# Optimization experiments

Hardware: AMD Instinct MI355X
Metric: run time of the kernel (lower is better)

The kernel has to match this reference:

```python
import jax, jax.numpy as jnp
import numpy as np


def setup_inputs() -> dict:
    key = jax.random.key(0)
    ks = jax.random.split(key, 5)
    b, t, q_dim, kv_dim, h = 16, 128, 256, 64, 4
    c = t - 1
    q_x = jax.random.normal(ks[0], (b, t, q_dim), dtype=jnp.float32)
    kv_x = jax.random.normal(ks[1], (b, t, c, kv_dim), dtype=jnp.float32)
    # Linear weights stored as [in, out]; no biases (bias=False in torch module).
    sq = 1.0 / np.sqrt(q_dim)
    sk = 1.0 / np.sqrt(kv_dim)
    Wq = jax.random.uniform(ks[2], (q_dim, kv_dim * h), jnp.float32, -sq, sq)
    Wk = jax.random.uniform(ks[3], (kv_dim, kv_dim * h), jnp.float32, -sk, sk)
    Wv = jax.random.uniform(ks[4], (kv_dim, kv_dim * h), jnp.float32, -sk, sk)
    return {"q_x": q_x, "kv_x": kv_x, "Wq": Wq, "Wk": Wk, "Wv": Wv}


def reference(q_x, kv_x, Wq, Wk, Wv):
    b, t, c, k = kv_x.shape  # c = t - 1
    h = Wq.shape[1] // k
    # projections
    q = (q_x @ Wq).reshape(b, t, h, k)          # [b,t,h,k]
    keys = (kv_x @ Wk).reshape(b, t, c, h, k)   # [b,t,c,h,k]
    vals = (kv_x @ Wv).reshape(b, t, c, h, k)
    # per-token attention over the c-sized context
    scores = jnp.einsum('bthk,btchk->bthc', q, keys) / jnp.sqrt(jnp.float32(k))
    w = jax.nn.softmax(scores, axis=-1)          # softmax over context dim
    out = jnp.einsum('bthc,btchk->bthk', w, vals)
    return out.reshape(b, t, h * k)
```

## Files before the change

### kernel.cpp

```cpp
#include <hip/hip_runtime.h>
#include <math.h>

#define Bdim 16
#define Tdim 128
#define Cdim 127
#define Hdim 4
#define QD   256
#define HK   256

#define DPP_XOR1        0xB1
#define DPP_XOR2        0x4E
#define DPP_HALF_MIRROR 0x141
#define DPP_MIRROR      0x140
template<int CTRL>
__device__ __forceinline__ float dpp_movf(float x) {
    return __int_as_float(__builtin_amdgcn_update_dpp(
        0, __float_as_int(x), CTRL, 0xF, 0xF, true));
}

__global__ __launch_bounds__(256) void precompute_M(
        const float* __restrict__ Wq, const float* __restrict__ Wk,
        float* __restrict__ M) {
    __shared__ float wk_s[64][129];
    __shared__ float wq_s[2][128];
    int I = blockIdx.x;
    int H = blockIdx.y;
    int tid = threadIdx.x;

    #pragma unroll
    for (int it = 0; it < 8; ++it) {
        int flat = tid + it * 256;
        int m = flat >> 5, kq = flat & 31;
        float4 v = *(const float4*)(Wk + m * HK + H * 128 + kq * 4);
        wk_s[m][kq*4+0] = v.x; wk_s[m][kq*4+1] = v.y;
        wk_s[m][kq*4+2] = v.z; wk_s[m][kq*4+3] = v.w;
    }
    if (tid < 64) {
        int r = tid >> 5, kq = tid & 31;
        float4 v = *(const float4*)(Wq + (size_t)(I*2+r) * HK + H * 128 + kq * 4);
        wq_s[r][kq*4+0] = v.x; wq_s[r][kq*4+1] = v.y;
        wq_s[r][kq*4+2] = v.z; wq_s[r][kq*4+3] = v.w;
    }
    __syncthreads();

    int r = tid >> 7, hh = (tid >> 6) & 1, m = tid & 63;
    float acc = 0.f;
    #pragma unroll 8
    for (int j = 0; j < 64; ++j)
        acc = fmaf(wq_s[r][hh*64+j], wk_s[m][hh*64+j], acc);
    M[(size_t)(I*2+r) * HK + H * 128 + hh * 64 + m] = acc;
}

template <int NS>
__global__ __launch_bounds__(256) void qk_gemm(
        const float* __restrict__ q_x,
        const float* __restrict__ M,
        float* __restrict__ part) {
    const int KLEN = 256 / NS;
    __shared__ __align__(16) float q_s[16][256 / NS];
    int RB = blockIdx.x;
    int S  = blockIdx.y;
    int tid = threadIdx.x;

    for (int f = tid; f < 16 * KLEN / 4; f += 256) {
        int r = f / (KLEN / 4), kq = f % (KLEN / 4);
        *(float4*)&q_s[r][kq*4] =
            *(const float4*)(q_x + (size_t)(RB*16 + r) * QD + S * KLEN + kq * 4);
    }
    __syncthreads();

    float acc[16];
    #pragma unroll
    for (int r = 0; r < 16; ++r) acc[r] = 0.f;

    for (int kk = 0; kk < KLEN / 4; ++kk) {
        int k = S * KLEN + kk * 4;
        float m0 = M[(size_t)(k+0) * HK + tid];
        float m1 = M[(size_t)(k+1) * HK + tid];
        float m2 = M[(size_t)(k+2) * HK + tid];
        float m3 = M[(size_t)(k+3) * HK + tid];
        #pragma unroll
        for (int r = 0; r < 16; ++r) {
            float4 qv = *(const float4*)&q_s[r][kk*4];
            acc[r] = fmaf(qv.x, m0, fmaf(qv.y, m1, fmaf(qv.z, m2, fmaf(qv.w, m3, acc[r]))));
        }
    }
    float* dst = part + (size_t)S * (Bdim*Tdim*HK) + (size_t)RB * 16 * HK + tid;
    #pragma unroll
    for (int r = 0; r < 16; ++r) dst[r * HK] = acc[r];
}

__global__ __launch_bounds__(512, 8) void attn_main(
        const float* __restrict__ kv_x,
        const float* __restrict__ qk_p, int nsplit,
        const float* __restrict__ Wv,
        float* __restrict__ out) {
    __shared__ __align__(16) float4 sX4[128 * 16];
    __shared__ __align__(16) float qk_s[HK];
    __shared__ __align__(16) float e_lds[128 * 5 + 4];
    __shared__ __align__(16) float4 wx4[Hdim * 16];
    __shared__ float red_max[Hdim][2];
    __shared__ float red_sum[Hdim][2];

    int bt  = blockIdx.x;
    int tid = threadIdx.x;

    const float4* Xg = (const float4*)(kv_x + (size_t)bt * (Cdim * 64));
    #pragma unroll
    for (int it = 0; it < 4; ++it) {
        int l = tid + it * 512;
        if (l < Cdim * 16) {
            int c = l >> 4, p = l & 15;
            __builtin_amdgcn_global_load_lds(
                (const __attribute__((address_space(1))) void*)(Xg + (c << 4) + (p ^ (c & 7))),
                (__attribute__((address_space(3))) void*)(sX4 + l), 16, 0, 0);
        }
    }
    if (tid >= 256 && tid < 320)
        ((float*)sX4)[Cdim * 64 + (tid - 256)] = 0.f;
    if (tid < 256) {
        float q = 0.f;
        for (int s = 0; s < nsplit; ++s)
            q += qk_p[(size_t)s * (Bdim*Tdim*HK) + (size_t)bt * HK + tid];
        qk_s[tid] = q;
    }
    __syncthreads();

    int h    = tid >> 7;
    int c    = tid & 127;
    int half = (tid >> 6) & 1;
    int lane = tid & 63;
    int sw   = c & 7;

    float s;
    {
        const float4* qrow = (const float4*)(qk_s + h * 64);
        const float4* xrow = sX4 + c * 16;
        float acc = 0.f;
        #pragma unroll
        for (int p = 0; p < 16; ++p) {
            float4 qv = qrow[p];
            float4 x4 = xrow[p ^ sw];
            acc = fmaf(qv.x, x4.x, fmaf(qv.y, x4.y, fmaf(qv.z, x4.z, fmaf(qv.w, x4.w, acc))));
        }
        s = (c < Cdim) ? acc * 0.125f : -INFINITY;
    }

    float mx = s;
    mx = fmaxf(mx, dpp_movf<DPP_XOR1>(mx));
    mx = fmaxf(mx, dpp_movf<DPP_XOR2>(mx));
    mx = fmaxf(mx, dpp_movf<DPP_HALF_MIRROR>(mx));
    mx = fmaxf(mx, dpp_movf<DPP_MIRROR>(mx));
    mx = fmaxf(mx, __shfl_xor(mx, 16, 64));
    mx = fmaxf(mx, __shfl_xor(mx, 32, 64));
    if (lane == 0) red_max[h][half] = mx;
    __syncthreads();
    float gm = fmaxf(red_max[h][0], red_max[h][1]);
    float e = __expf(s - gm);
    e_lds[c * 5 + h] = e;
    float sm = e;
    sm += dpp_movf<DPP_XOR1>(sm);
    sm += dpp_movf<DPP_XOR2>(sm);
    sm += dpp_movf<DPP_HALF_MIRROR>(sm);
    sm += dpp_movf<DPP_MIRROR>(sm);
    sm += __shfl_xor(sm, 16, 64);
    sm += __shfl_xor(sm, 32, 64);
    if (lane == 0) red_sum[h][half] = sm;
    __syncthreads();

    {
        int jc = (tid >> 3) & 15;
        int cs = tid & 7;
        const float4* xbase = sX4 + cs * 16 + (jc ^ cs);
        const float* ebase  = e_lds + cs * 5 + h;
        float4 a = {0.f, 0.f, 0.f, 0.f};
        #pragma unroll
        for (int m = 0; m < 16; ++m) {
            float4 x4 = xbase[m * 128];
            float ev  = ebase[m * 40];
            a.x = fmaf(ev, x4.x, a.x);
            a.y = fmaf(ev, x4.y, a.y);
            a.z = fmaf(ev, x4.z, a.z);
            a.w = fmaf(ev, x4.w, a.w);
        }
        a.x += dpp_movf<DPP_XOR1>(a.x); a.y += dpp_movf<DPP_XOR1>(a.y);
        a.z += dpp_movf<DPP_XOR1>(a.z); a.w += dpp_movf<DPP_XOR1>(a.w);
        a.x += dpp_movf<DPP_XOR2>(a.x); a.y += dpp_movf<DPP_XOR2>(a.y);
        a.z += dpp_movf<DPP_XOR2>(a.z); a.w += dpp_movf<DPP_XOR2>(a.w);
        a.x += dpp_movf<DPP_HALF_MIRROR>(a.x); a.y += dpp_movf<DPP_HALF_MIRROR>(a.y);
        a.z += dpp_movf<DPP_HALF_MIRROR>(a.z); a.w += dpp_movf<DPP_HALF_MIRROR>(a.w);
        if (cs == 0) wx4[h * 16 + jc] = a;
    }
    __syncthreads();

    if (tid < 256) {
        int hh = tid >> 6, k = tid & 63;
        float inv = 1.f / (red_sum[hh][0] + red_sum[hh][1]);
        const float* wvcol = Wv + hh * 64 + k;
        float acc = 0.f;
        #pragma unroll 4
        for (int jc = 0; jc < 16; ++jc) {
            float4 w4 = wx4[hh * 16 + jc];
            acc = fmaf(w4.x, wvcol[(size_t)(jc*4+0) * HK], acc);
            acc = fmaf(w4.y, wvcol[(size_t)(jc*4+1) * HK], acc);
            acc = fmaf(w4.z, wvcol[(size_t)(jc*4+2) * HK], acc);
            acc = fmaf(w4.w, wvcol[(size_t)(jc*4+3) * HK], acc);
        }
        out[(size_t)bt * HK + tid] = acc * inv;
    }
}

extern "C" void kernel_launch(void* const* d_in, const int* in_sizes, int n_in,
                              void* d_out, int out_size, void* d_ws, size_t ws_size,
                              hipStream_t stream) {
    const float* q_x  = (const float*)d_in[0];
    const float* kv_x = (const float*)d_in[1];
    const float* Wq   = (const float*)d_in[2];
    const float* Wk   = (const float*)d_in[3];
    const float* Wv   = (const float*)d_in[4];
    float* out = (float*)d_out;

    float* M     = (float*)d_ws;
    float* parts = M + 256 * 256;

    size_t need4 = (size_t)(256*256 + 4 * Bdim*Tdim*HK) * sizeof(float);
    int nsplit = (ws_size >= need4) ? 4 : 1;

    precompute_M<<<dim3(128, 2), 256, 0, stream>>>(Wq, Wk, M);
    if (nsplit == 4)
        qk_gemm<4><<<dim3(128, 4), 256, 0, stream>>>(q_x, M, parts);
    else
        qk_gemm<1><<<dim3(128, 1), 256, 0, stream>>>(q_x, M, parts);
    attn_main<<<Bdim * Tdim, 512, 0, stream>>>(kv_x, parts, nsplit, Wv, out);
}
```

Before: 42.05 us.

## Make attention blocks persistent over four tokens with double-buffered LDS prefetch

Each attention block now handles four consecutive (b,t) tokens and prefetches the next token's kv_x tile into a second LDS buffer while it computes the current one. The qk partial sums are prefetched into registers. The upper 256 threads keep their Wv column in 64 registers across iterations, so Wv is read once per block. The goal is to hide global-load latency, amortise Wv loads and cut the block count. The costs are higher register use (launch bounds drop to 4 blocks), double the LDS footprint, manual waitcnt/barrier scheduling that is fragile, and fewer blocks (512), which may leave CUs underfilled.

```diff
diff --git a/kernel.cpp b/kernel.cpp
--- a/kernel.cpp
+++ b/kernel.cpp
@@ -7,6 +7,9 @@
 #define Hdim 4
 #define QD   256
 #define HK   256
+#define BT   (Bdim * Tdim)
+#define ITERS 4
+#define NBLK  (BT / ITERS)
 
 #define DPP_XOR1        0xB1
 #define DPP_XOR2        0x4E
@@ -85,46 +88,57 @@
             acc[r] = fmaf(qv.x, m0, fmaf(qv.y, m1, fmaf(qv.z, m2, fmaf(qv.w, m3, acc[r]))));
         }
     }
-    float* dst = part + (size_t)S * (Bdim*Tdim*HK) + (size_t)RB * 16 * HK + tid;
+    float* dst = part + (size_t)S * (BT*HK) + (size_t)RB * 16 * HK + tid;
     #pragma unroll
     for (int r = 0; r < 16; ++r) dst[r * HK] = acc[r];
 }
 
-__global__ __launch_bounds__(512, 8) void attn_main(
+__device__ __forceinline__ void stage_x(const float4* __restrict__ Xg,
+                                        float4* dst, int tid) {
+    #pragma unroll
+    for (int itr = 0; itr < 4; ++itr) {
+        int l = tid + itr * 512;
+        int c = l >> 4, p = l & 15;
+        int src = (l < Cdim * 16) ? ((c << 4) + (p ^ (c & 7))) : 0;
+        __builtin_amdgcn_global_load_lds(
+            (const __attribute__((address_space(1))) void*)(Xg + src),
+            (__attribute__((address_space(3))) void*)(dst + l), 16, 0, 0);
+    }
+}
+
+template <int NS>
+__global__ __launch_bounds__(512, 4) void attn_main(
         const float* __restrict__ kv_x,
-        const float* __restrict__ qk_p, int nsplit,
+        const float* __restrict__ qk_p,
         const float* __restrict__ Wv,
         float* __restrict__ out) {
-    __shared__ __align__(16) float4 sX4[128 * 16];
-    __shared__ __align__(16) float qk_s[HK];
+    __shared__ __align__(16) float4 sX[2 * 2048];
+    __shared__ __align__(16) float qk_s[2][HK];
     __shared__ __align__(16) float e_lds[128 * 5 + 4];
     __shared__ __align__(16) float4 wx4[Hdim * 16];
     __shared__ float red_max[Hdim][2];
     __shared__ float red_sum[Hdim][2];
 
-    int bt  = blockIdx.x;
+    int blk = blockIdx.x;
     int tid = threadIdx.x;
-
-    const float4* Xg = (const float4*)(kv_x + (size_t)bt * (Cdim * 64));
-    #pragma unroll
-    for (int it = 0; it < 4; ++it) {
-        int l = tid + it * 512;
-        if (l < Cdim * 16) {
-            int c = l >> 4, p = l & 15;
-            __builtin_amdgcn_global_load_lds(
-                (const __attribute__((address_space(1))) void*)(Xg + (c << 4) + (p ^ (c & 7))),
-                (__attribute__((address_space(3))) void*)(sX4 + l), 16, 0, 0);
-        }
-    }
-    if (tid >= 256 && tid < 320)
-        ((float*)sX4)[Cdim * 64 + (tid - 256)] = 0.f;
-    if (tid < 256) {
-        float q = 0.f;
-        for (int s = 0; s < nsplit; ++s)
-            q += qk_p[(size_t)s * (Bdim*Tdim*HK) + (size_t)bt * HK + tid];
-        qk_s[tid] = q;
-    }
-    __syncthreads();
+    bool hiw = (tid >= 256);
+    int bt0 = blk * ITERS;
+
+    float wv[64];
+    if (hiw) {
+        int col = tid & 255;
+        #pragma unroll
+        for (int j = 0; j < 64; ++j) wv[j] = Wv[(size_t)j * HK + col];
+    }
+
+    stage_x((const float4*)(kv_x + (size_t)bt0 * (Cdim * 64)), sX, tid);
+    __builtin_amdgcn_sched_barrier(0);
+    float r[NS];
+    if (!hiw) {
+        #pragma unroll
+        for (int s = 0; s < NS; ++s)
+            r[s] = qk_p[(size_t)s * (BT*HK) + (size_t)bt0 * HK + tid];
+    }
 
     int h    = tid >> 7;
     int c    = tid & 127;
@@ -132,81 +146,120 @@
     int lane = tid & 63;
     int sw   = c & 7;
 
-    float s;
-    {
-        const float4* qrow = (const float4*)(qk_s + h * 64);
-        const float4* xrow = sX4 + c * 16;
-        float acc = 0.f;
-        #pragma unroll
-        for (int p = 0; p < 16; ++p) {
-            float4 qv = qrow[p];
-            float4 x4 = xrow[p ^ sw];
-            acc = fmaf(qv.x, x4.x, fmaf(qv.y, x4.y, fmaf(qv.z, x4.z, fmaf(qv.w, x4.w, acc))));
-        }
-        s = (c < Cdim) ? acc * 0.125f : -INFINITY;
-    }
-
-    float mx = s;
-    mx = fmaxf(mx, dpp_movf<DPP_XOR1>(mx));
-    mx = fmaxf(mx, dpp_movf<DPP_XOR2>(mx));
-    mx = fmaxf(mx, dpp_movf<DPP_HALF_MIRROR>(mx));
-    mx = fmaxf(mx, dpp_movf<DPP_MIRROR>(mx));
-    mx = fmaxf(mx, __shfl_xor(mx, 16, 64));
-    mx = fmaxf(mx, __shfl_xor(mx, 32, 64));
-    if (lane == 0) red_max[h][half] = mx;
-    __syncthreads();
-    float gm = fmaxf(red_max[h][0], red_max[h][1]);
-    float e = __expf(s - gm);
-    e_lds[c * 5 + h] = e;
-    float sm = e;
-    sm += dpp_movf<DPP_XOR1>(sm);
-    sm += dpp_movf<DPP_XOR2>(sm);
-    sm += dpp_movf<DPP_HALF_MIRROR>(sm);
-    sm += dpp_movf<DPP_MIRROR>(sm);
-    sm += __shfl_xor(sm, 16, 64);
-    sm += __shfl_xor(sm, 32, 64);
-    if (lane == 0) red_sum[h][half] = sm;
-    __syncthreads();
-
-    {
-        int jc = (tid >> 3) & 15;
-        int cs = tid & 7;
-        const float4* xbase = sX4 + cs * 16 + (jc ^ cs);
-        const float* ebase  = e_lds + cs * 5 + h;
-        float4 a = {0.f, 0.f, 0.f, 0.f};
-        #pragma unroll
-        for (int m = 0; m < 16; ++m) {
-            float4 x4 = xbase[m * 128];
-            float ev  = ebase[m * 40];
-            a.x = fmaf(ev, x4.x, a.x);
-            a.y = fmaf(ev, x4.y, a.y);
-            a.z = fmaf(ev, x4.z, a.z);
-            a.w = fmaf(ev, x4.w, a.w);
-        }
-        a.x += dpp_movf<DPP_XOR1>(a.x); a.y += dpp_movf<DPP_XOR1>(a.y);
-        a.z += dpp_movf<DPP_XOR1>(a.z); a.w += dpp_movf<DPP_XOR1>(a.w);
-        a.x += dpp_movf<DPP_XOR2>(a.x); a.y += dpp_movf<DPP_XOR2>(a.y);
-        a.z += dpp_movf<DPP_XOR2>(a.z); a.w += dpp_movf<DPP_XOR2>(a.w);
-        a.x += dpp_movf<DPP_HALF_MIRROR>(a.x); a.y += dpp_movf<DPP_HALF_MIRROR>(a.y);
-        a.z += dpp_movf<DPP_HALF_MIRROR>(a.z); a.w += dpp_movf<DPP_HALF_MIRROR>(a.w);
-        if (cs == 0) wx4[h * 16 + jc] = a;
-    }
-    __syncthreads();
-
-    if (tid < 256) {
-        int hh = tid >> 6, k = tid & 63;
-        float inv = 1.f / (red_sum[hh][0] + red_sum[hh][1]);
-        const float* wvcol = Wv + hh * 64 + k;
-        float acc = 0.f;
-        #pragma unroll 4
-        for (int jc = 0; jc < 16; ++jc) {
-            float4 w4 = wx4[hh * 16 + jc];
-            acc = fmaf(w4.x, wvcol[(size_t)(jc*4+0) * HK], acc);
-            acc = fmaf(w4.y, wvcol[(size_t)(jc*4+1) * HK], acc);
-            acc = fmaf(w4.z, wvcol[(size_t)(jc*4+2) * HK], acc);
-            acc = fmaf(w4.w, wvcol[(size_t)(jc*4+3) * HK], acc);
-        }
-        out[(size_t)bt * HK + tid] = acc * inv;
+    for (int it = 0; it < ITERS; ++it) {
+        int cur = it & 1;
+        int bt = bt0 + it;
+        bool have_nxt = (it + 1 < ITERS);
+
+        __builtin_amdgcn_s_barrier();
+        __builtin_amdgcn_sched_barrier(0);
+
+        if (have_nxt)
+            stage_x((const float4*)(kv_x + (size_t)(bt+1) * (Cdim * 64)),
+                    sX + (cur ^ 1) * 2048, tid);
+        __builtin_amdgcn_sched_barrier(0);
+
+        if (!hiw) {
+            float qsum = 0.f;
+            #pragma unroll
+            for (int s = 0; s < NS; ++s) qsum += r[s];
+            if (have_nxt) {
+                #pragma unroll
+                for (int s = 0; s < NS; ++s)
+                    r[s] = qk_p[(size_t)s * (BT*HK) + (size_t)(bt+1) * HK + tid];
+            }
+            qk_s[cur][tid] = qsum;
+            asm volatile("s_waitcnt lgkmcnt(0)" ::: "memory");
+        } else {
+            if (have_nxt) asm volatile("s_waitcnt vmcnt(4)" ::: "memory");
+            else          asm volatile("s_waitcnt vmcnt(0)" ::: "memory");
+        }
+        __builtin_amdgcn_s_barrier();
+        __builtin_amdgcn_sched_barrier(0);
+
+        float s;
+        {
+            const float4* qrow = (const float4*)(qk_s[cur] + h * 64);
+            const float4* xrow = sX + cur * 2048 + c * 16;
+            float acc = 0.f;
+            #pragma unroll
+            for (int p = 0; p < 16; ++p) {
+                float4 qv = qrow[p];
+                float4 x4 = xrow[p ^ sw];
+                acc = fmaf(qv.x, x4.x, fmaf(qv.y, x4.y, fmaf(qv.z, x4.z, fmaf(qv.w, x4.w, acc))));
+            }
+            s = (c < Cdim) ? acc * 0.125f : -INFINITY;
+        }
+
+        float mx = s;
+        mx = fmaxf(mx, dpp_movf<DPP_XOR1>(mx));
+        mx = fmaxf(mx, dpp_movf<DPP_XOR2>(mx));
+        mx = fmaxf(mx, dpp_movf<DPP_HALF_MIRROR>(mx));
+        mx = fmaxf(mx, dpp_movf<DPP_MIRROR>(mx));
+        mx = fmaxf(mx, __shfl_xor(mx, 16, 64));
+        mx = fmaxf(mx, __shfl_xor(mx, 32, 64));
+        if (lane == 0) red_max[h][half] = mx;
+        asm volatile("s_waitcnt lgkmcnt(0)" ::: "memory");
+        __builtin_amdgcn_s_barrier();
+        __builtin_amdgcn_sched_barrier(0);
+
+        float gm = fmaxf(red_max[h][0], red_max[h][1]);
+        float e = __expf(s - gm);
+        e_lds[c * 5 + h] = e;
+        float sm = e;
+        sm += dpp_movf<DPP_XOR1>(sm);
+        sm += dpp_movf<DPP_XOR2>(sm);
+        sm += dpp_movf<DPP_HALF_MIRROR>(sm);
+        sm += dpp_movf<DPP_MIRROR>(sm);
+        sm += __shfl_xor(sm, 16, 64);
+        sm += __shfl_xor(sm, 32, 64);
+        if (lane == 0) red_sum[h][half] = sm;
+        asm volatile("s_waitcnt lgkmcnt(0)" ::: "memory");
+        __builtin_amdgcn_s_barrier();
+        __builtin_amdgcn_sched_barrier(0);
+
+        {
+            int jc = (tid >> 3) & 15;
+            int cs = tid & 7;
+            const float4* xbase = sX + cur * 2048 + cs * 16 + (jc ^ cs);
+            const float* ebase  = e_lds + cs * 5 + h;
+            float4 a = {0.f, 0.f, 0.f, 0.f};
+            #pragma unroll
+            for (int m = 0; m < 16; ++m) {
+                float4 x4 = xbase[m * 128];
+                float ev  = ebase[m * 40];
+                a.x = fmaf(ev, x4.x, a.x);
+                a.y = fmaf(ev, x4.y, a.y);
+                a.z = fmaf(ev, x4.z, a.z);
+                a.w = fmaf(ev, x4.w, a.w);
+            }
+            a.x += dpp_movf<DPP_XOR1>(a.x); a.y += dpp_movf<DPP_XOR1>(a.y);
+            a.z += dpp_movf<DPP_XOR1>(a.z); a.w += dpp_movf<DPP_XOR1>(a.w);
+            a.x += dpp_movf<DPP_XOR2>(a.x); a.y += dpp_movf<DPP_XOR2>(a.y);
+            a.z += dpp_movf<DPP_XOR2>(a.z); a.w += dpp_movf<DPP_XOR2>(a.w);
+            a.x += dpp_movf<DPP_HALF_MIRROR>(a.x); a.y += dpp_movf<DPP_HALF_MIRROR>(a.y);
+            a.z += dpp_movf<DPP_HALF_MIRROR>(a.z); a.w += dpp_movf<DPP_HALF_MIRROR>(a.w);
+            if (cs == 0) wx4[h * 16 + jc] = a;
+        }
+        asm volatile("s_waitcnt lgkmcnt(0)" ::: "memory");
+        __builtin_amdgcn_s_barrier();
+        __builtin_amdgcn_sched_barrier(0);
+
+        if (hiw) {
+            int col = tid & 255;
+            int hh = col >> 6;
+            float inv = 1.f / (red_sum[hh][0] + red_sum[hh][1]);
+            float acc = 0.f;
+            #pragma unroll
+            for (int jc = 0; jc < 16; ++jc) {
+                float4 w4 = wx4[hh * 16 + jc];
+                acc = fmaf(w4.x, wv[jc*4+0],
+                      fmaf(w4.y, wv[jc*4+1],
+                      fmaf(w4.z, wv[jc*4+2],
+                      fmaf(w4.w, wv[jc*4+3], acc))));
+            }
+            out[(size_t)bt * HK + col] = acc * inv;
+        }
     }
 }
 
@@ -223,13 +276,15 @@
     float* M     = (float*)d_ws;
     float* parts = M + 256 * 256;
 
-    size_t need4 = (size_t)(256*256 + 4 * Bdim*Tdim*HK) * sizeof(float);
+    size_t need4 = (size_t)(256*256 + 4 * BT*HK) * sizeof(float);
     int nsplit = (ws_size >= need4) ? 4 : 1;
 
     precompute_M<<<dim3(128, 2), 256, 0, stream>>>(Wq, Wk, M);
-    if (nsplit == 4)
+    if (nsplit == 4) {
         qk_gemm<4><<<dim3(128, 4), 256, 0, stream>>>(q_x, M, parts);
-    else
+        attn_main<4><<<NBLK, 512, 0, stream>>>(kv_x, parts, Wv, out);
+    } else {
         qk_gemm<1><<<dim3(128, 1), 256, 0, stream>>>(q_x, M, parts);
-    attn_main<<<Bdim * Tdim, 512, 0, stream>>>(kv_x, parts, nsplit, Wv, out);
-}
+        attn_main<1><<<NBLK, 512, 0, stream>>>(kv_x, parts, Wv, out);
+    }
+}
```

New measurement: 65.90 us. 1.57x slower.

## Remap attention threads so each loads context row once for all heads

Applied to the files above, without the earlier changes.

Changes the score computation in attn_main so four threads share one context row and each computes partial dots for all four heads. The row is read from LDS once instead of once per head, and a quad DPP reduction finishes each dot. The weighted-sum stage now keeps four heads' accumulators per thread, reusing each X load across heads, and the softmax max/sum are stored as float4 per wave. The split count becomes a template parameter and the launch bound drops from 8 to 6 blocks per CU. In exchange the kernel uses more registers and does more cross-lane reductions.

```diff
diff --git a/kernel.cpp b/kernel.cpp
--- a/kernel.cpp
+++ b/kernel.cpp
@@ -7,6 +7,7 @@
 #define Hdim 4
 #define QD   256
 #define HK   256
+#define BT   (Bdim * Tdim)
 
 #define DPP_XOR1        0xB1
 #define DPP_XOR2        0x4E
@@ -16,6 +17,33 @@
 __device__ __forceinline__ float dpp_movf(float x) {
     return __int_as_float(__builtin_amdgcn_update_dpp(
         0, __float_as_int(x), CTRL, 0xF, 0xF, true));
+}
+__device__ __forceinline__ float quad_sum(float v) {
+    v += dpp_movf<DPP_XOR1>(v);
+    v += dpp_movf<DPP_XOR2>(v);
+    return v;
+}
+__device__ __forceinline__ float rows_max(float v) {
+    v = fmaxf(v, dpp_movf<DPP_HALF_MIRROR>(v));
+    v = fmaxf(v, dpp_movf<DPP_MIRROR>(v));
+    v = fmaxf(v, __shfl_xor(v, 16, 64));
+    v = fmaxf(v, __shfl_xor(v, 32, 64));
+    return v;
+}
+__device__ __forceinline__ float rows_sum(float v) {
+    v += dpp_movf<DPP_HALF_MIRROR>(v);
+    v += dpp_movf<DPP_MIRROR>(v);
+    v += __shfl_xor(v, 16, 64);
+    v += __shfl_xor(v, 32, 64);
+    return v;
+}
+__device__ __forceinline__ float wx_red(float v) {
+    v += dpp_movf<DPP_XOR1>(v);
+    v += dpp_movf<DPP_XOR2>(v);
+    v += dpp_movf<DPP_HALF_MIRROR>(v);
+    v += dpp_movf<DPP_MIRROR>(v);
+    v += __shfl_xor(v, 16, 64);
+    return v;
 }
 
 __global__ __launch_bounds__(256) void precompute_M(
@@ -85,22 +113,23 @@
             acc[r] = fmaf(qv.x, m0, fmaf(qv.y, m1, fmaf(qv.z, m2, fmaf(qv.w, m3, acc[r]))));
         }
     }
-    float* dst = part + (size_t)S * (Bdim*Tdim*HK) + (size_t)RB * 16 * HK + tid;
+    float* dst = part + (size_t)S * (BT*HK) + (size_t)RB * 16 * HK + tid;
     #pragma unroll
     for (int r = 0; r < 16; ++r) dst[r * HK] = acc[r];
 }
 
-__global__ __launch_bounds__(512, 8) void attn_main(
+template <int NS>
+__global__ __launch_bounds__(512, 6) void attn_main(
         const float* __restrict__ kv_x,
-        const float* __restrict__ qk_p, int nsplit,
+        const float* __restrict__ qk_p,
         const float* __restrict__ Wv,
         float* __restrict__ out) {
     __shared__ __align__(16) float4 sX4[128 * 16];
     __shared__ __align__(16) float qk_s[HK];
-    __shared__ __align__(16) float e_lds[128 * 5 + 4];
+    __shared__ __align__(16) float4 e4[128];
     __shared__ __align__(16) float4 wx4[Hdim * 16];
-    __shared__ float red_max[Hdim][2];
-    __shared__ float red_sum[Hdim][2];
+    __shared__ __align__(16) float4 redm[8];
+    __shared__ __align__(16) float4 reds[8];
 
     int bt  = blockIdx.x;
     int tid = threadIdx.x;
@@ -120,91 +149,119 @@
         ((float*)sX4)[Cdim * 64 + (tid - 256)] = 0.f;
     if (tid < 256) {
         float q = 0.f;
-        for (int s = 0; s < nsplit; ++s)
-            q += qk_p[(size_t)s * (Bdim*Tdim*HK) + (size_t)bt * HK + tid];
+        #pragma unroll
+        for (int s = 0; s < NS; ++s)
+            q += qk_p[(size_t)s * (BT*HK) + (size_t)bt * HK + tid];
         qk_s[tid] = q;
     }
     __syncthreads();
 
-    int h    = tid >> 7;
-    int c    = tid & 127;
-    int half = (tid >> 6) & 1;
     int lane = tid & 63;
-    int sw   = c & 7;
-
-    float s;
+    int wave = tid >> 6;
+    int c  = tid >> 2;
+    int qp = tid & 3;
+    int sw = c & 7;
+
+    float s0, s1, s2, s3;
     {
-        const float4* qrow = (const float4*)(qk_s + h * 64);
         const float4* xrow = sX4 + c * 16;
-        float acc = 0.f;
-        #pragma unroll
-        for (int p = 0; p < 16; ++p) {
-            float4 qv = qrow[p];
-            float4 x4 = xrow[p ^ sw];
-            acc = fmaf(qv.x, x4.x, fmaf(qv.y, x4.y, fmaf(qv.z, x4.z, fmaf(qv.w, x4.w, acc))));
-        }
-        s = (c < Cdim) ? acc * 0.125f : -INFINITY;
-    }
-
-    float mx = s;
-    mx = fmaxf(mx, dpp_movf<DPP_XOR1>(mx));
-    mx = fmaxf(mx, dpp_movf<DPP_XOR2>(mx));
-    mx = fmaxf(mx, dpp_movf<DPP_HALF_MIRROR>(mx));
-    mx = fmaxf(mx, dpp_movf<DPP_MIRROR>(mx));
-    mx = fmaxf(mx, __shfl_xor(mx, 16, 64));
-    mx = fmaxf(mx, __shfl_xor(mx, 32, 64));
-    if (lane == 0) red_max[h][half] = mx;
-    __syncthreads();
-    float gm = fmaxf(red_max[h][0], red_max[h][1]);
-    float e = __expf(s - gm);
-    e_lds[c * 5 + h] = e;
-    float sm = e;
-    sm += dpp_movf<DPP_XOR1>(sm);
-    sm += dpp_movf<DPP_XOR2>(sm);
-    sm += dpp_movf<DPP_HALF_MIRROR>(sm);
-    sm += dpp_movf<DPP_MIRROR>(sm);
-    sm += __shfl_xor(sm, 16, 64);
-    sm += __shfl_xor(sm, 32, 64);
-    if (lane == 0) red_sum[h][half] = sm;
+        float4 x0 = xrow[(qp*4 + 0) ^ sw];
+        float4 x1 = xrow[(qp*4 + 1) ^ sw];
+        float4 x2 = xrow[(qp*4 + 2) ^ sw];
+        float4 x3 = xrow[(qp*4 + 3) ^ sw];
+        const float4* qk4 = (const float4*)qk_s;
+        float a0 = 0.f, a1 = 0.f, a2 = 0.f, a3 = 0.f;
+        #pragma unroll
+        for (int i = 0; i < 4; ++i) {
+            float4 xi = (i == 0) ? x0 : (i == 1) ? x1 : (i == 2) ? x2 : x3;
+            float4 q0 = qk4[0*16 + qp*4 + i];
+            float4 q1 = qk4[1*16 + qp*4 + i];
+            float4 q2 = qk4[2*16 + qp*4 + i];
+            float4 q3 = qk4[3*16 + qp*4 + i];
+            a0 = fmaf(q0.x, xi.x, fmaf(q0.y, xi.y, fmaf(q0.z, xi.z, fmaf(q0.w, xi.w, a0))));
+            a1 = fmaf(q1.x, xi.x, fmaf(q1.y, xi.y, fmaf(q1.z, xi.z, fmaf(q1.w, xi.w, a1))));
+            a2 = fmaf(q2.x, xi.x, fmaf(q2.y, xi.y, fmaf(q2.z, xi.z, fmaf(q2.w, xi.w, a2))));
+            a3 = fmaf(q3.x, xi.x, fmaf(q3.y, xi.y, fmaf(q3.z, xi.z, fmaf(q3.w, xi.w, a3))));
+        }
+        a0 = quad_sum(a0); a1 = quad_sum(a1); a2 = quad_sum(a2); a3 = quad_sum(a3);
+        bool valid = (c < Cdim);
+        s0 = valid ? a0 * 0.125f : -INFINITY;
+        s1 = valid ? a1 * 0.125f : -INFINITY;
+        s2 = valid ? a2 * 0.125f : -INFINITY;
+        s3 = valid ? a3 * 0.125f : -INFINITY;
+    }
+
+    float m0 = rows_max(s0), m1 = rows_max(s1), m2 = rows_max(s2), m3 = rows_max(s3);
+    if (lane == 0) redm[wave] = make_float4(m0, m1, m2, m3);
+    __syncthreads();
+    float4 gm = redm[0];
+    #pragma unroll
+    for (int w = 1; w < 8; ++w) {
+        float4 r = redm[w];
+        gm.x = fmaxf(gm.x, r.x); gm.y = fmaxf(gm.y, r.y);
+        gm.z = fmaxf(gm.z, r.z); gm.w = fmaxf(gm.w, r.w);
+    }
+    float e0 = __expf(s0 - gm.x);
+    float e1 = __expf(s1 - gm.y);
+    float e2 = __expf(s2 - gm.z);
+    float e3 = __expf(s3 - gm.w);
+    if (qp == 0) e4[c] = make_float4(e0, e1, e2, e3);
+    float t0 = rows_sum(e0), t1 = rows_sum(e1), t2 = rows_sum(e2), t3 = rows_sum(e3);
+    if (lane == 0) reds[wave] = make_float4(t0, t1, t2, t3);
     __syncthreads();
 
     {
-        int jc = (tid >> 3) & 15;
-        int cs = tid & 7;
-        const float4* xbase = sX4 + cs * 16 + (jc ^ cs);
-        const float* ebase  = e_lds + cs * 5 + h;
-        float4 a = {0.f, 0.f, 0.f, 0.f};
-        #pragma unroll
-        for (int m = 0; m < 16; ++m) {
-            float4 x4 = xbase[m * 128];
-            float ev  = ebase[m * 40];
-            a.x = fmaf(ev, x4.x, a.x);
-            a.y = fmaf(ev, x4.y, a.y);
-            a.z = fmaf(ev, x4.z, a.z);
-            a.w = fmaf(ev, x4.w, a.w);
-        }
-        a.x += dpp_movf<DPP_XOR1>(a.x); a.y += dpp_movf<DPP_XOR1>(a.y);
-        a.z += dpp_movf<DPP_XOR1>(a.z); a.w += dpp_movf<DPP_XOR1>(a.w);
-        a.x += dpp_movf<DPP_XOR2>(a.x); a.y += dpp_movf<DPP_XOR2>(a.y);
-        a.z += dpp_movf<DPP_XOR2>(a.z); a.w += dpp_movf<DPP_XOR2>(a.w);
-        a.x += dpp_movf<DPP_HALF_MIRROR>(a.x); a.y += dpp_movf<DPP_HALF_MIRROR>(a.y);
-        a.z += dpp_movf<DPP_HALF_MIRROR>(a.z); a.w += dpp_movf<DPP_HALF_MIRROR>(a.w);
-        if (cs == 0) wx4[h * 16 + jc] = a;
+        int jc = tid >> 5;
+        int mq = (lane >> 3) & 3;
+        int cs = lane & 7;
+        float4 A0 = {0,0,0,0}, A1 = {0,0,0,0}, A2 = {0,0,0,0}, A3 = {0,0,0,0};
+        #pragma unroll
+        for (int mm = 0; mm < 4; ++mm) {
+            int cc = cs + 8 * (mq * 4 + mm);
+            float4 x4 = sX4[cc * 16 + (jc ^ cs)];
+            float4 ee = e4[cc];
+            A0.x = fmaf(ee.x, x4.x, A0.x); A0.y = fmaf(ee.x, x4.y, A0.y);
+            A0.z = fmaf(ee.x, x4.z, A0.z); A0.w = fmaf(ee.x, x4.w, A0.w);
+            A1.x = fmaf(ee.y, x4.x, A1.x); A1.y = fmaf(ee.y, x4.y, A1.y);
+            A1.z = fmaf(ee.y, x4.z, A1.z); A1.w = fmaf(ee.y, x4.w, A1.w);
+            A2.x = fmaf(ee.z, x4.x, A2.x); A2.y = fmaf(ee.z, x4.y, A2.y);
+            A2.z = fmaf(ee.z, x4.z, A2.z); A2.w = fmaf(ee.z, x4.w, A2.w);
+            A3.x = fmaf(ee.w, x4.x, A3.x); A3.y = fmaf(ee.w, x4.y, A3.y);
+            A3.z = fmaf(ee.w, x4.z, A3.z); A3.w = fmaf(ee.w, x4.w, A3.w);
+        }
+        A0.x = wx_red(A0.x); A0.y = wx_red(A0.y); A0.z = wx_red(A0.z); A0.w = wx_red(A0.w);
+        A1.x = wx_red(A1.x); A1.y = wx_red(A1.y); A1.z = wx_red(A1.z); A1.w = wx_red(A1.w);
+        A2.x = wx_red(A2.x); A2.y = wx_red(A2.y); A2.z = wx_red(A2.z); A2.w = wx_red(A2.w);
+        A3.x = wx_red(A3.x); A3.y = wx_red(A3.y); A3.z = wx_red(A3.z); A3.w = wx_red(A3.w);
+        if ((lane & 31) == 0) {
+            wx4[0 * 16 + jc] = A0;
+            wx4[1 * 16 + jc] = A1;
+            wx4[2 * 16 + jc] = A2;
+            wx4[3 * 16 + jc] = A3;
+        }
     }
     __syncthreads();
 
     if (tid < 256) {
         int hh = tid >> 6, k = tid & 63;
-        float inv = 1.f / (red_sum[hh][0] + red_sum[hh][1]);
+        float4 sums = reds[0];
+        #pragma unroll
+        for (int w = 1; w < 8; ++w) {
+            float4 r = reds[w];
+            sums.x += r.x; sums.y += r.y; sums.z += r.z; sums.w += r.w;
+        }
+        float denom = (hh == 0) ? sums.x : (hh == 1) ? sums.y
+                    : (hh == 2) ? sums.z : sums.w;
+        float inv = 1.f / denom;
         const float* wvcol = Wv + hh * 64 + k;
         float acc = 0.f;
         #pragma unroll 4
         for (int jc = 0; jc < 16; ++jc) {
             float4 w4 = wx4[hh * 16 + jc];
-            acc = fmaf(w4.x, wvcol[(size_t)(jc*4+0) * HK], acc);
-            acc = fmaf(w4.y, wvcol[(size_t)(jc*4+1) * HK], acc);
-            acc = fmaf(w4.z, wvcol[(size_t)(jc*4+2) * HK], acc);
-            acc = fmaf(w4.w, wvcol[(size_t)(jc*4+3) * HK], acc);
+            acc = fmaf(w4.x, wvcol[(size_t)(jc*4+0) * HK],
+                  fmaf(w4.y, wvcol[(size_t)(jc*4+1) * HK],
+                  fmaf(w4.z, wvcol[(size_t)(jc*4+2) * HK],
+                  fmaf(w4.w, wvcol[(size_t)(jc*4+3) * HK], acc))));
         }
         out[(size_t)bt * HK + tid] = acc * inv;
     }
@@ -223,13 +280,15 @@
     float* M     = (float*)d_ws;
     float* parts = M + 256 * 256;
 
-    size_t need4 = (size_t)(256*256 + 4 * Bdim*Tdim*HK) * sizeof(float);
+    size_t need4 = (size_t)(256*256 + 4 * BT*HK) * sizeof(float);
     int nsplit = (ws_size >= need4) ? 4 : 1;
 
     precompute_M<<<dim3(128, 2), 256, 0, stream>>>(Wq, Wk, M);
-    if (nsplit == 4)
+    if (nsplit == 4) {
         qk_gemm<4><<<dim3(128, 4), 256, 0, stream>>>(q_x, M, parts);
-    else
+        attn_main<4><<<BT, 512, 0, stream>>>(kv_x, parts, Wv, out);
+    } else {
         qk_gemm<1><<<dim3(128, 1), 256, 0, stream>>>(q_x, M, parts);
-    attn_main<<<Bdim * Tdim, 512, 0, stream>>>(kv_x, parts, nsplit, Wv, out);
-}
+        attn_main<1><<<BT, 512, 0, stream>>>(kv_x, parts, Wv, out);
+    }
+}
```

Measured after the change: 42.46 us. No clear change (+1.0%).
